# Kernel tuning notes

Measured on AMD Instinct MI355X. Metric: run time of the kernel, lower is better.

## Reference

```python
import jax, jax.numpy as jnp
import numpy as np

N = 100000
E = 1600000
IN_C = 128
HID = 128


def setup_inputs() -> dict:
    key = jax.random.key(0)
    ks = jax.random.split(key, 16)
    x = jax.random.normal(ks[0], (N, IN_C), dtype=jnp.float32)
    edge_index = jax.random.randint(ks[1], (2, E), 0, N, dtype=jnp.int64)

    def lin(k, fan_in, fan_out):
        kw, kb = jax.random.split(k)
        bound = 1.0 / np.sqrt(fan_in)
        w = jax.random.uniform(kw, (fan_in, fan_out), minval=-bound, maxval=bound, dtype=jnp.float32)
        b = jax.random.uniform(kb, (fan_out,), minval=-bound, maxval=bound, dtype=jnp.float32)
        return w, b

    w0a, b0a = lin(ks[2], IN_C, HID)
    w0b, b0b = lin(ks[3], HID, HID)
    w1a, b1a = lin(ks[4], HID, HID)
    w1b, b1b = lin(ks[5], HID, HID)
    w2a, b2a = lin(ks[6], HID, HID)
    w2b, b2b = lin(ks[7], HID, HID)
    lin_w, lin_b = lin(ks[8], HID, 1)
    return {
        "x": x, "edge_index": edge_index,
        "w0a": w0a, "b0a": b0a, "w0b": w0b, "b0b": b0b,
        "w1a": w1a, "b1a": b1a, "w1b": w1b, "b1b": b1b,
        "w2a": w2a, "b2a": b2a, "w2b": w2b, "b2b": b2b,
        "lin_w": lin_w, "lin_b": lin_b,
    }


def _gin_conv(x, src, dst, wa, ba, wb, bb):
    # scatter-add neighbor sum: agg[i] = sum_{(j,i) in edges} x[j]  (eps = 0)
    agg = jax.ops.segment_sum(x[src], dst, num_segments=N)
    h = x + agg
    h = jax.nn.relu(h @ wa + ba)
    return h @ wb + bb


def reference(x, edge_index, w0a, b0a, w0b, b0b, w1a, b1a, w1b, b1b,
              w2a, b2a, w2b, b2b, lin_w, lin_b):
    src, dst = edge_index[0], edge_index[1]
    # dropout is identity in eval mode
    h = jax.nn.elu(_gin_conv(x, src, dst, w0a, b0a, w0b, b0b))
    h = jax.nn.elu(_gin_conv(h, src, dst, w1a, b1a, w1b, b1b))
    h = jax.nn.elu(_gin_conv(h, src, dst, w2a, b2a, w2b, b2b))
    out = jax.nn.sigmoid(h @ lin_w + lin_b)
    return out.squeeze(-1)  # [N]
```

## Files before the change

kernel.cpp:

```cpp
#include <hip/hip_runtime.h>
#include <hip/hip_bf16.h>
#include <math.h>

#define NN 100000
#define CC 128
#define EE 1600000
#define EPT 8
#define FCHUNK (256 * EPT)
#define NCHUNKS ((EE + FCHUNK - 1) / FCHUNK)
#define NB_E NCHUNKS
#define WB 512
#define WSHIFT 9
#define NBUCK ((NN + WB - 1) / WB)

typedef short  bf16x8 __attribute__((ext_vector_type(8)));
typedef float  f32x4  __attribute__((ext_vector_type(4)));
typedef float  f32x4v __attribute__((ext_vector_type(4)));
typedef unsigned short u16x8 __attribute__((ext_vector_type(8)));

#define WPAD 136
#define TP   136
#define MLPB 256
#define MLPW 16

__device__ __forceinline__ ushort f2bf(float f) {
    __hip_bfloat16 h = __float2bfloat16(f);
    return __builtin_bit_cast(ushort, h);
}
__device__ __forceinline__ float bf2f(ushort u) {
    return __builtin_bit_cast(float, ((unsigned int)u) << 16);
}


__global__ void __launch_bounds__(256) bucket_hist(
    const int* __restrict__ dst, int* __restrict__ cnt)
{
    __shared__ int h[NBUCK];
    for (int i = threadIdx.x; i < NBUCK; i += 256) h[i] = 0;
    __syncthreads();
    int base = blockIdx.x * FCHUNK + threadIdx.x * EPT;
    if (base + EPT <= EE) {
        int4 d0 = *(const int4*)&dst[base];
        int4 d1 = *(const int4*)&dst[base + 4];
        int dd[8] = {d0.x, d0.y, d0.z, d0.w, d1.x, d1.y, d1.z, d1.w};
#pragma unroll
        for (int i = 0; i < 8; ++i) atomicAdd(&h[dd[i] >> WSHIFT], 1);
    } else {
        for (int i = 0; i < EPT; ++i) {
            int e = base + i;
            if (e < EE) atomicAdd(&h[dst[e] >> WSHIFT], 1);
        }
    }
    __syncthreads();
    for (int i = threadIdx.x; i < NBUCK; i += 256)
        cnt[i * NB_E + blockIdx.x] = h[i];
}

__global__ void __launch_bounds__(256) scan_cnt(
    int* __restrict__ cnt, int* __restrict__ total)
{
    __shared__ int wsum[4];
    int row = blockIdx.x;
    int* p = cnt + row * NB_E;
    int tid = threadIdx.x, lane = tid & 63, wid = tid >> 6;
    int v[4], s = 0;
#pragma unroll
    for (int j = 0; j < 4; ++j) {
        int idx = tid * 4 + j;
        v[j] = (idx < NB_E) ? p[idx] : 0;
        s += v[j];
    }
    int inc = s;
#pragma unroll
    for (int off = 1; off < 64; off <<= 1) {
        int n = __shfl_up(inc, off);
        if (lane >= off) inc += n;
    }
    if (lane == 63) wsum[wid] = inc;
    __syncthreads();
    int wofs = 0;
#pragma unroll
    for (int w = 0; w < 4; ++w)
        if (w < wid) wofs += wsum[w];
    int run = wofs + inc - s;
#pragma unroll
    for (int j = 0; j < 4; ++j) {
        int idx = tid * 4 + j;
        if (idx < NB_E) p[idx] = run;
        run += v[j];
    }
    if (tid == 255) total[row] = run;
}

__global__ void scan_base(const int* __restrict__ total,
                          int* __restrict__ bucketBase, int* __restrict__ rowptr)
{
    int lane = threadIdx.x;
    int v[4], s = 0;
#pragma unroll
    for (int j = 0; j < 4; ++j) {
        int idx = lane * 4 + j;
        v[j] = (idx < NBUCK) ? total[idx] : 0;
        s += v[j];
    }
    int inc = s;
#pragma unroll
    for (int off = 1; off < 64; off <<= 1) {
        int n = __shfl_up(inc, off);
        if (lane >= off) inc += n;
    }
    int run = inc - s;
#pragma unroll
    for (int j = 0; j < 4; ++j) {
        int idx = lane * 4 + j;
        if (idx < NBUCK) bucketBase[idx] = run;
        run += v[j];
    }
    if (lane == 63) { bucketBase[NBUCK] = EE; rowptr[NN] = EE; }
}

__global__ void __launch_bounds__(256) bucket_scatter(
    const int* __restrict__ src, const int* __restrict__ dst,
    const int* __restrict__ cntEx, const int* __restrict__ bucketBase,
    unsigned int* __restrict__ pairs)
{
    __shared__ int h[NBUCK];
    __shared__ int bOfs[NBUCK];
    for (int i = threadIdx.x; i < NBUCK; i += 256) {
        h[i] = 0;
        bOfs[i] = bucketBase[i] + cntEx[i * NB_E + blockIdx.x];
    }
    __syncthreads();
    int base = blockIdx.x * FCHUNK + threadIdx.x * EPT;
    if (base + EPT <= EE) {
        int4 d0 = *(const int4*)&dst[base];
        int4 d1 = *(const int4*)&dst[base + 4];
        int4 s0 = *(const int4*)&src[base];
        int4 s1 = *(const int4*)&src[base + 4];
        int dd[8] = {d0.x, d0.y, d0.z, d0.w, d1.x, d1.y, d1.z, d1.w};
        int ss[8] = {s0.x, s0.y, s0.z, s0.w, s1.x, s1.y, s1.z, s1.w};
#pragma unroll
        for (int i = 0; i < 8; ++i) {
            int d = dd[i];
            int k = d >> WSHIFT;
            int r = atomicAdd(&h[k], 1);
            pairs[bOfs[k] + r] = ((unsigned)ss[i] << WSHIFT) | (unsigned)(d & (WB - 1));
        }
    } else {
        for (int i = 0; i < EPT; ++i) {
            int e = base + i;
            if (e < EE) {
                int d = dst[e];
                int k = d >> WSHIFT;
                int r = atomicAdd(&h[k], 1);
                pairs[bOfs[k] + r] = ((unsigned)src[e] << WSHIFT) | (unsigned)(d & (WB - 1));
            }
        }
    }
}

__global__ void __launch_bounds__(256) csr_build(
    const unsigned int* __restrict__ pairs, const int* __restrict__ bucketBase,
    int* __restrict__ rowptr, int* __restrict__ col)
{
    __shared__ int cnt[WB];
    __shared__ int ofs[WB];
    __shared__ int wsum[4];
    int k = blockIdx.x;
    int tid = threadIdx.x, lane = tid & 63, wid = tid >> 6;
    int nodeBase = k * WB;
    int nNodes = NN - nodeBase; if (nNodes > WB) nNodes = WB;
    for (int i = tid; i < WB; i += 256) cnt[i] = 0;
    __syncthreads();
    int beg = bucketBase[k], end = bucketBase[k + 1];
    for (int e = beg + tid; e < end; e += 256)
        atomicAdd(&cnt[pairs[e] & (WB - 1)], 1);
    __syncthreads();
    int a = cnt[2 * tid], b = cnt[2 * tid + 1];
    int s = a + b;
    int inc = s;
#pragma unroll
    for (int off = 1; off < 64; off <<= 1) {
        int n = __shfl_up(inc, off);
        if (lane >= off) inc += n;
    }
    if (lane == 63) wsum[wid] = inc;
    __syncthreads();
    int wofs = 0;
#pragma unroll
    for (int w = 0; w < 4; ++w)
        if (w < wid) wofs += wsum[w];
    int excl = wofs + inc - s;
    ofs[2 * tid] = excl;
    ofs[2 * tid + 1] = excl + a;
    __syncthreads();
    for (int i = tid; i < nNodes; i += 256)
        rowptr[nodeBase + i] = beg + ofs[i];
    __syncthreads();
    for (int e = beg + tid; e < end; e += 256) {
        unsigned p = pairs[e];
        int dl = p & (WB - 1);
        int r = atomicAdd(&ofs[dl], 1);
        col[beg + r] = (int)(p >> WSHIFT);
    }
}

__global__ void __launch_bounds__(256) convert_x_kernel(
    const float* __restrict__ x, ushort* __restrict__ xb)
{
    int i = blockIdx.x * 256 + threadIdx.x;
    f32x4v v = __builtin_nontemporal_load((const f32x4v*)x + i);
    ushort4 o;
    o.x = f2bf(v[0]); o.y = f2bf(v[1]); o.z = f2bf(v[2]); o.w = f2bf(v[3]);
    ((ushort4*)xb)[i] = o;
}

__global__ void __launch_bounds__(256) convert_w6_kernel(
    const float* __restrict__ w0, const float* __restrict__ w1,
    const float* __restrict__ w2, const float* __restrict__ w3,
    const float* __restrict__ w4, const float* __restrict__ w5,
    ushort* __restrict__ wt)
{
    int i = blockIdx.x * 256 + threadIdx.x;
    int mat = i >> 14;
    int rem = i & 16383;
    int k = rem >> 7, n = rem & 127;
    const float* w = (mat == 0) ? w0 : (mat == 1) ? w1 : (mat == 2) ? w2
                   : (mat == 3) ? w3 : (mat == 4) ? w4 : w5;
    wt[mat * 16384 + n * 128 + k] = f2bf(w[k * 128 + n]);
}

__global__ void __launch_bounds__(256) gather_agg(
    const ushort* __restrict__ hin, const int* __restrict__ rowptr,
    const int* __restrict__ col, ushort* __restrict__ agg)
{
    const int grp    = threadIdx.x >> 4;
    const int lane16 = threadIdx.x & 15;
    const int gbase  = (threadIdx.x & 63) & 48;
    const int n = blockIdx.x * 16 + grp;
    const u16x8* hp = (const u16x8*)hin;

    u16x8 self = hp[n * 16 + lane16];
    float s0[8], s1[8], s2[8], s3[8];
#pragma unroll
    for (int k = 0; k < 8; ++k) {
        s0[k] = bf2f(self[k]); s1[k] = 0.f; s2[k] = 0.f; s3[k] = 0.f;
    }

    int beg = rowptr[n], end = rowptr[n + 1];
    while (beg < end) {
        int take = end - beg;
        if (take > 16) take = 16;
        int ci = (lane16 < take) ? col[beg + lane16] : 0;
        int j = 0;
        for (; j + 4 <= take; j += 4) {
            int n0 = __shfl(ci, gbase + j + 0);
            int n1 = __shfl(ci, gbase + j + 1);
            int n2 = __shfl(ci, gbase + j + 2);
            int n3 = __shfl(ci, gbase + j + 3);
            u16x8 a0 = hp[n0 * 16 + lane16];
            u16x8 a1 = hp[n1 * 16 + lane16];
            u16x8 a2 = hp[n2 * 16 + lane16];
            u16x8 a3 = hp[n3 * 16 + lane16];
#pragma unroll
            for (int k = 0; k < 8; ++k) {
                s0[k] += bf2f(a0[k]); s1[k] += bf2f(a1[k]);
                s2[k] += bf2f(a2[k]); s3[k] += bf2f(a3[k]);
            }
        }
        for (; j < take; ++j) {
            int n0 = __shfl(ci, gbase + j);
            u16x8 a0 = hp[n0 * 16 + lane16];
#pragma unroll
            for (int k = 0; k < 8; ++k) s0[k] += bf2f(a0[k]);
        }
        beg += take;
    }

    bf16x8 o;
#pragma unroll
    for (int k = 0; k < 8; ++k) o[k] = (short)f2bf(s0[k] + s1[k] + s2[k] + s3[k]);
    *(bf16x8*)&((ushort*)agg)[n * CC + lane16 * 8] = o;
}

template <bool FUSE_HEAD>
__global__ void __launch_bounds__(1024, 2) mlp_persist(
    const ushort* __restrict__ hin,
    const ushort* __restrict__ waT, const float* __restrict__ ba,
    const ushort* __restrict__ wbT, const float* __restrict__ bb,
    ushort* __restrict__ hout,
    const float* __restrict__ lw, const float* __restrict__ lb,
    float* __restrict__ out)
{
    __shared__ ushort WaS[CC * WPAD];
    __shared__ ushort WbS[CC * WPAD];
    __shared__ ushort Tt[MLPW][16 * TP];
    __shared__ float  baS[CC], bbS[CC], lwS[CC];

    const int tid = threadIdx.x;

    for (int i = tid; i < CC * 16; i += 1024) {
        int row = i >> 4, ch = i & 15;
        *(bf16x8*)&WaS[row * WPAD + ch * 8] = *(const bf16x8*)&waT[row * CC + ch * 8];
        *(bf16x8*)&WbS[row * WPAD + ch * 8] = *(const bf16x8*)&wbT[row * CC + ch * 8];
    }
    if (tid < CC)                       baS[tid]           = ba[tid];
    else if (tid < 2 * CC)              bbS[tid - CC]      = bb[tid - CC];
    else if (FUSE_HEAD && tid < 3 * CC) lwS[tid - 2 * CC]  = lw[tid - 2 * CC];
    __syncthreads();

    const int wave = tid >> 6;
    const int lane = tid & 63;
    const int quad = lane >> 4;
    const int l16  = lane & 15;
    ushort* T = Tt[wave];
    const int nTiles = NN / 16;
    const int stride = MLPB * MLPW;
    const int fq4 = quad * 4;
    float lbv = FUSE_HEAD ? lb[0] : 0.f;
    ushort* Trow = &T[l16 * TP];

    for (int wv = blockIdx.x * MLPW + wave; wv < nTiles; wv += stride) {
        const int wrow0 = wv * 16;

        bf16x8 af[4];
#pragma unroll
        for (int kk = 0; kk < 4; ++kk)
            af[kk] = *(const bf16x8*)&hin[(wrow0 + l16) * CC + kk * 32 + quad * 8];

#pragma unroll
        for (int nt = 0; nt < 8; ++nt) {
            f32x4 a = *(const f32x4*)&baS[nt * 16 + fq4];
#pragma unroll
            for (int kk = 0; kk < 4; ++kk) {
                bf16x8 wfrag = *(const bf16x8*)&WaS[(nt * 16 + l16) * WPAD + kk * 32 + quad * 8];
                a = __builtin_amdgcn_mfma_f32_16x16x32_bf16(wfrag, af[kk], a, 0, 0, 0);
            }
            ushort4 pk;
            pk.x = f2bf(fmaxf(a[0], 0.f));
            pk.y = f2bf(fmaxf(a[1], 0.f));
            pk.z = f2bf(fmaxf(a[2], 0.f));
            pk.w = f2bf(fmaxf(a[3], 0.f));
            *(ushort4*)&Trow[nt * 16 + fq4] = pk;
        }
        __builtin_amdgcn_sched_barrier(0);

        bf16x8 tf[4];
#pragma unroll
        for (int kk = 0; kk < 4; ++kk)
            tf[kk] = *(const bf16x8*)&Trow[kk * 32 + quad * 8];
        __builtin_amdgcn_sched_barrier(0);

        if (FUSE_HEAD) {
            float part = 0.f;
#pragma unroll
            for (int nt = 0; nt < 8; ++nt) {
                f32x4 a2 = *(const f32x4*)&bbS[nt * 16 + fq4];
#pragma unroll
                for (int kk = 0; kk < 4; ++kk) {
                    bf16x8 wfrag = *(const bf16x8*)&WbS[(nt * 16 + l16) * WPAD + kk * 32 + quad * 8];
                    a2 = __builtin_amdgcn_mfma_f32_16x16x32_bf16(wfrag, tf[kk], a2, 0, 0, 0);
                }
                f32x4 lw4 = *(const f32x4*)&lwS[nt * 16 + fq4];
#pragma unroll
                for (int r = 0; r < 4; ++r) {
                    float v = a2[r];
                    v = v > 0.f ? v : expm1f(v);
                    part += v * lw4[r];
                }
            }
            part += __shfl_xor(part, 16);
            part += __shfl_xor(part, 32);
            if (lane < 16) {
                float z = part + lbv;
                out[wrow0 + l16] = 1.f / (1.f + expf(-z));
            }
        } else {
#pragma unroll
            for (int nt = 0; nt < 8; ++nt) {
                f32x4 a2 = *(const f32x4*)&bbS[nt * 16 + fq4];
#pragma unroll
                for (int kk = 0; kk < 4; ++kk) {
                    bf16x8 wfrag = *(const bf16x8*)&WbS[(nt * 16 + l16) * WPAD + kk * 32 + quad * 8];
                    a2 = __builtin_amdgcn_mfma_f32_16x16x32_bf16(wfrag, tf[kk], a2, 0, 0, 0);
                }
                ushort4 pk;
#pragma unroll
                for (int r = 0; r < 4; ++r) {
                    float v = a2[r];
                    v = v > 0.f ? v : expm1f(v);
                    ((ushort*)&pk)[r] = f2bf(v);
                }
                *(ushort4*)&Trow[nt * 16 + fq4] = pk;
            }
#pragma unroll
            for (int i = 0; i < 4; ++i) {
                int r = i * 4 + quad;
                bf16x8 o = *(const bf16x8*)&T[r * TP + l16 * 8];
                *(bf16x8*)&hout[(wrow0 + r) * CC + l16 * 8] = o;
            }
        }
    }
}

extern "C" void kernel_launch(void* const* d_in, const int* in_sizes, int n_in,
                              void* d_out, int out_size, void* d_ws, size_t ws_size,
                              hipStream_t stream) {
    const float* x   = (const float*)d_in[0];
    const int*   ei  = (const int*)d_in[1];
    const int*   src = ei;
    const int*   dst = ei + EE;
    const float* w0a = (const float*)d_in[2];
    const float* b0a = (const float*)d_in[3];
    const float* w0b = (const float*)d_in[4];
    const float* b0b = (const float*)d_in[5];
    const float* w1a = (const float*)d_in[6];
    const float* b1a = (const float*)d_in[7];
    const float* w1b = (const float*)d_in[8];
    const float* b1b = (const float*)d_in[9];
    const float* w2a = (const float*)d_in[10];
    const float* b2a = (const float*)d_in[11];
    const float* w2b = (const float*)d_in[12];
    const float* b2b = (const float*)d_in[13];
    const float* lw  = (const float*)d_in[14];
    const float* lb  = (const float*)d_in[15];
    float* outp = (float*)d_out;

    ushort* xb  = (ushort*)d_ws;
    ushort* hbA = xb + (size_t)NN * CC;
    ushort* agg = hbA + (size_t)NN * CC;
    ushort* wT  = agg + (size_t)NN * CC;
    int* col    = (int*)(wT + 6 * CC * CC);
    int* rowptr = col + EE;

    unsigned int* pairs = (unsigned int*)agg;
    int* cnt        = (int*)(pairs + EE);
    int* total      = cnt + NBUCK * NB_E;
    int* bucketBase = total + NBUCK;

    ushort* w0aT = wT;
    ushort* w0bT = wT + 1 * CC * CC;
    ushort* w1aT = wT + 2 * CC * CC;
    ushort* w1bT = wT + 3 * CC * CC;
    ushort* w2aT = wT + 4 * CC * CC;
    ushort* w2bT = wT + 5 * CC * CC;

    const int gatherBlocks = NN / 16;
    const int cvtXBlocks   = (NN * CC / 4) / 256;

    convert_x_kernel<<<cvtXBlocks, 256, 0, stream>>>(x, xb);
    convert_w6_kernel<<<6 * 64, 256, 0, stream>>>(w0a, w0b, w1a, w1b, w2a, w2b, wT);

    bucket_hist<<<NB_E, 256, 0, stream>>>(dst, cnt);
    scan_cnt<<<NBUCK, 256, 0, stream>>>(cnt, total);
    scan_base<<<1, 64, 0, stream>>>(total, bucketBase, rowptr);
    bucket_scatter<<<NB_E, 256, 0, stream>>>(src, dst, cnt, bucketBase, pairs);
    csr_build<<<NBUCK, 256, 0, stream>>>(pairs, bucketBase, rowptr, col);

    gather_agg<<<gatherBlocks, 256, 0, stream>>>(xb, rowptr, col, agg);
    mlp_persist<false><<<MLPB, 1024, 0, stream>>>(agg, w0aT, b0a, w0bT, b0b, hbA,
                                                  nullptr, nullptr, nullptr);
    gather_agg<<<gatherBlocks, 256, 0, stream>>>(hbA, rowptr, col, agg);
    mlp_persist<false><<<MLPB, 1024, 0, stream>>>(agg, w1aT, b1a, w1bT, b1b, xb,
                                                  nullptr, nullptr, nullptr);
    gather_agg<<<gatherBlocks, 256, 0, stream>>>(xb, rowptr, col, agg);
    mlp_persist<true><<<MLPB, 1024, 0, stream>>>(agg, w2aT, b2a, w2bT, b2b, nullptr,
                                                 lw, lb, outp);
}
```

Baseline: 403.8 us.

## Slice feature matrices into 16-channel planes for cache-local neighbor gather

Stores bf16 node features as 8 separate slices of 16 channels (32 bytes per node) instead of row-major 256-byte rows. The gather kernel now launches one block per node group per slice, with pairs of lanes splitting neighbors and reducing via shuffles, so each slice's working set (about 3.2 MB) fits in cache during the random gather. The convert and MLP kernels are updated to read and write the sliced layout. The cost is eight times more gather blocks, repeated rowptr/col reads per slice, and extra shuffle reductions, plus 32-byte granularity accesses that may underuse cache lines.

```diff
diff --git a/kernel.cpp b/kernel.cpp
--- a/kernel.cpp
+++ b/kernel.cpp
@@ -12,10 +12,11 @@
 #define WB 512
 #define WSHIFT 9
 #define NBUCK ((NN + WB - 1) / WB)
+#define NSLICE 8
+#define SL ((size_t)NN * 16)
 
 typedef short  bf16x8 __attribute__((ext_vector_type(8)));
 typedef float  f32x4  __attribute__((ext_vector_type(4)));
-typedef float  f32x4v __attribute__((ext_vector_type(4)));
 typedef unsigned short u16x8 __attribute__((ext_vector_type(8)));
 
 #define WPAD 136
@@ -208,11 +209,19 @@
 __global__ void __launch_bounds__(256) convert_x_kernel(
     const float* __restrict__ x, ushort* __restrict__ xb)
 {
-    int i = blockIdx.x * 256 + threadIdx.x;
-    f32x4v v = __builtin_nontemporal_load((const f32x4v*)x + i);
-    ushort4 o;
-    o.x = f2bf(v[0]); o.y = f2bf(v[1]); o.z = f2bf(v[2]); o.w = f2bf(v[3]);
-    ((ushort4*)xb)[i] = o;
+    int t = blockIdx.x * 256 + threadIdx.x;
+    int n = t >> 4;
+    int c = t & 15;
+    int s = c >> 1, h = c & 1;
+    const float* xp = &x[n * CC + s * 16 + h * 8];
+    f32x4 f0 = __builtin_nontemporal_load((const f32x4*)xp);
+    f32x4 f1 = __builtin_nontemporal_load((const f32x4*)(xp + 4));
+    bf16x8 o;
+    o[0] = (short)f2bf(f0[0]); o[1] = (short)f2bf(f0[1]);
+    o[2] = (short)f2bf(f0[2]); o[3] = (short)f2bf(f0[3]);
+    o[4] = (short)f2bf(f1[0]); o[5] = (short)f2bf(f1[1]);
+    o[6] = (short)f2bf(f1[2]); o[7] = (short)f2bf(f1[3]);
+    *(bf16x8*)&xb[(size_t)s * SL + (size_t)n * 16 + h * 8] = o;
 }
 
 __global__ void __launch_bounds__(256) convert_w6_kernel(
@@ -230,57 +239,75 @@
     wt[mat * 16384 + n * 128 + k] = f2bf(w[k * 128 + n]);
 }
 
-__global__ void __launch_bounds__(256) gather_agg(
-    const ushort* __restrict__ hin, const int* __restrict__ rowptr,
-    const int* __restrict__ col, ushort* __restrict__ agg)
-{
-    const int grp    = threadIdx.x >> 4;
-    const int lane16 = threadIdx.x & 15;
-    const int gbase  = (threadIdx.x & 63) & 48;
-    const int n = blockIdx.x * 16 + grp;
-    const u16x8* hp = (const u16x8*)hin;
-
-    u16x8 self = hp[n * 16 + lane16];
-    float s0[8], s1[8], s2[8], s3[8];
-#pragma unroll
-    for (int k = 0; k < 8; ++k) {
-        s0[k] = bf2f(self[k]); s1[k] = 0.f; s2[k] = 0.f; s3[k] = 0.f;
-    }
-
-    int beg = rowptr[n], end = rowptr[n + 1];
+__global__ void __launch_bounds__(256) gather_slice(
+    const ushort* __restrict__ hs, const int* __restrict__ rowptr,
+    const int* __restrict__ col, ushort* __restrict__ aggs)
+{
+    const int s     = blockIdx.x & (NSLICE - 1);
+    const int nb    = blockIdx.x >> 3;
+    const int grp   = threadIdx.x >> 4;
+    const int l16   = threadIdx.x & 15;
+    const int pair  = l16 >> 1;
+    const int half  = l16 & 1;
+    const int gbase = (threadIdx.x & 63) & 48;
+    const int n = nb * 16 + grp;
+    const ushort* base = hs + (size_t)s * SL;
+
+    u16x8 self = *(const u16x8*)&base[(size_t)n * 16 + half * 8];
+    float s0[8], s1[8];
+#pragma unroll
+    for (int k = 0; k < 8; ++k) { s0[k] = 0.f; s1[k] = 0.f; }
+
+    int beg = __builtin_nontemporal_load(&rowptr[n]);
+    int end = __builtin_nontemporal_load(&rowptr[n + 1]);
     while (beg < end) {
         int take = end - beg;
         if (take > 16) take = 16;
-        int ci = (lane16 < take) ? col[beg + lane16] : 0;
+        int ci = (l16 < take) ? __builtin_nontemporal_load(&col[beg + l16]) : 0;
         int j = 0;
-        for (; j + 4 <= take; j += 4) {
-            int n0 = __shfl(ci, gbase + j + 0);
-            int n1 = __shfl(ci, gbase + j + 1);
-            int n2 = __shfl(ci, gbase + j + 2);
-            int n3 = __shfl(ci, gbase + j + 3);
-            u16x8 a0 = hp[n0 * 16 + lane16];
-            u16x8 a1 = hp[n1 * 16 + lane16];
-            u16x8 a2 = hp[n2 * 16 + lane16];
-            u16x8 a3 = hp[n3 * 16 + lane16];
-#pragma unroll
-            for (int k = 0; k < 8; ++k) {
-                s0[k] += bf2f(a0[k]); s1[k] += bf2f(a1[k]);
-                s2[k] += bf2f(a2[k]); s3[k] += bf2f(a3[k]);
-            }
-        }
-        for (; j < take; ++j) {
-            int n0 = __shfl(ci, gbase + j);
-            u16x8 a0 = hp[n0 * 16 + lane16];
+        for (; j + 16 <= take; j += 16) {
+            int na = __shfl(ci, gbase + j + pair);
+            int nbx = __shfl(ci, gbase + j + 8 + pair);
+            u16x8 a0 = *(const u16x8*)&base[(size_t)na * 16 + half * 8];
+            u16x8 a1 = *(const u16x8*)&base[(size_t)nbx * 16 + half * 8];
+#pragma unroll
+            for (int k = 0; k < 8; ++k) { s0[k] += bf2f(a0[k]); s1[k] += bf2f(a1[k]); }
+        }
+        for (; j + 8 <= take; j += 8) {
+            int na = __shfl(ci, gbase + j + pair);
+            u16x8 a0 = *(const u16x8*)&base[(size_t)na * 16 + half * 8];
 #pragma unroll
             for (int k = 0; k < 8; ++k) s0[k] += bf2f(a0[k]);
         }
+        if (j < take) {
+            int m = take - j;
+            int idx = (pair < m) ? pair : 0;
+            int na = __shfl(ci, gbase + j + idx);
+            u16x8 a0 = *(const u16x8*)&base[(size_t)na * 16 + half * 8];
+            if (pair < m) {
+#pragma unroll
+                for (int k = 0; k < 8; ++k) s0[k] += bf2f(a0[k]);
+            }
+        }
         beg += take;
     }
 
-    bf16x8 o;
-#pragma unroll
-    for (int k = 0; k < 8; ++k) o[k] = (short)f2bf(s0[k] + s1[k] + s2[k] + s3[k]);
-    *(bf16x8*)&((ushort*)agg)[n * CC + lane16 * 8] = o;
+    float v[8];
+#pragma unroll
+    for (int k = 0; k < 8; ++k) {
+        float t = s0[k] + s1[k];
+        t += __shfl_xor(t, 2);
+        t += __shfl_xor(t, 4);
+        t += __shfl_xor(t, 8);
+        v[k] = t + bf2f(self[k]);
+    }
+
+    if (pair == 0) {
+        bf16x8 o;
+#pragma unroll
+        for (int k = 0; k < 8; ++k) o[k] = (short)f2bf(v[k]);
+        *(bf16x8*)&aggs[(size_t)s * SL + (size_t)n * 16 + half * 8] = o;
+    }
 }
 
 template <bool FUSE_HEAD>
@@ -326,7 +353,8 @@
         bf16x8 af[4];
 #pragma unroll
         for (int kk = 0; kk < 4; ++kk)
-            af[kk] = *(const bf16x8*)&hin[(wrow0 + l16) * CC + kk * 32 + quad * 8];
+            af[kk] = *(const bf16x8*)&hin[(size_t)(2 * kk + (quad >> 1)) * SL
+                                          + (size_t)(wrow0 + l16) * 16 + (quad & 1) * 8];
 
 #pragma unroll
         for (int nt = 0; nt < 8; ++nt) {
@@ -397,7 +425,8 @@
             for (int i = 0; i < 4; ++i) {
                 int r = i * 4 + quad;
                 bf16x8 o = *(const bf16x8*)&T[r * TP + l16 * 8];
-                *(bf16x8*)&hout[(wrow0 + r) * CC + l16 * 8] = o;
+                *(bf16x8*)&hout[(size_t)(l16 >> 1) * SL
+                                + (size_t)(wrow0 + r) * 16 + (l16 & 1) * 8] = o;
             }
         }
     }
@@ -445,25 +474,25 @@
     ushort* w2aT = wT + 4 * CC * CC;
     ushort* w2bT = wT + 5 * CC * CC;
 
-    const int gatherBlocks = NN / 16;
-    const int cvtXBlocks   = (NN * CC / 4) / 256;
+    const int gatherBlocks = (NN / 16) * NSLICE;
+    const int cvtXBlocks   = (NN * 16) / 256;
 
     convert_x_kernel<<<cvtXBlocks, 256, 0, stream>>>(x, xb);
     convert_w6_kernel<<<6 * 64, 256, 0, stream>>>(w0a, w0b, w1a, w1b, w2a, w2b, wT);
 
-    bucket_hist<<<NB_E, 256, 0, stream>>>(dst, cnt);
+    bucket_hist<<<NCHUNKS, 256, 0, stream>>>(dst, cnt);
     scan_cnt<<<NBUCK, 256, 0, stream>>>(cnt, total);
     scan_base<<<1, 64, 0, stream>>>(total, bucketBase, rowptr);
-    bucket_scatter<<<NB_E, 256, 0, stream>>>(src, dst, cnt, bucketBase, pairs);
+    bucket_scatter<<<NCHUNKS, 256, 0, stream>>>(src, dst, cnt, bucketBase, pairs);
     csr_build<<<NBUCK, 256, 0, stream>>>(pairs, bucketBase, rowptr, col);
 
-    gather_agg<<<gatherBlocks, 256, 0, stream>>>(xb, rowptr, col, agg);
+    gather_slice<<<gatherBlocks, 256, 0, stream>>>(xb, rowptr, col, agg);
     mlp_persist<false><<<MLPB, 1024, 0, stream>>>(agg, w0aT, b0a, w0bT, b0b, hbA,
                                                   nullptr, nullptr, nullptr);
-    gather_agg<<<gatherBlocks, 256, 0, stream>>>(hbA, rowptr, col, agg);
+    gather_slice<<<gatherBlocks, 256, 0, stream>>>(hbA, rowptr, col, agg);
     mlp_persist<false><<<MLPB, 1024, 0, stream>>>(agg, w1aT, b1a, w1bT, b1b, xb,
                                                   nullptr, nullptr, nullptr);
-    gather_agg<<<gatherBlocks, 256, 0, stream>>>(xb, rowptr, col, agg);
+    gather_slice<<<gatherBlocks, 256, 0, stream>>>(xb, rowptr, col, agg);
     mlp_persist<true><<<MLPB, 1024, 0, stream>>>(agg, w2aT, b2a, w2bT, b2b, nullptr,
                                                  lw, lb, outp);
 }
```

New measurement: 597.7 us. 1.48x slower.
